# Kernel tuning notes

Measured on AMD Instinct MI355X. Metric: run time of the kernel, lower is better.

The kernel has to match this reference:

```python
import jax, jax.numpy as jnp
import numpy as np

B, S, D, H = 2, 2048, 1024, 16
DEPTH = D // H


def setup_inputs() -> dict:
    key = jax.random.key(0)
    ks = jax.random.split(key, 6)
    q = jax.random.normal(ks[0], (B, S, D), dtype=jnp.float32)
    k = jax.random.normal(ks[1], (B, S, D), dtype=jnp.float32)
    v = jax.random.normal(ks[2], (B, S, D), dtype=jnp.float32)
    # causal mask, broadcastable to [B, H, S, S]
    mask = jnp.tril(jnp.ones((S, S), dtype=bool))[None, None, :, :]
    wq = jax.random.normal(ks[3], (D, D), dtype=jnp.float32)
    wk = jax.random.normal(ks[4], (D, D), dtype=jnp.float32)
    wv = jax.random.normal(ks[5], (D, D), dtype=jnp.float32)
    return {"q": q, "k": k, "v": v, "mask": mask, "wq": wq, "wk": wk, "wv": wv}


def _split_heads(x):
    # [B, S, D] -> [B, H, S, depth]
    return x.reshape(x.shape[0], -1, H, DEPTH).transpose(0, 2, 1, 3)


def reference(q, k, v, mask, wq, wk, wv):
    q = _split_heads(q @ wq)
    k = _split_heads(k @ wk)
    v = _split_heads(v @ wv)
    scale = jnp.sqrt(jnp.float32(DEPTH))
    # [B, H, S, S]
    scores = jnp.einsum("bhqd,bhkd->bhqk", q, k) / scale
    scores = jnp.where(mask, scores, jnp.float32(-8.0))
    scores = scores - jnp.max(scores, axis=-1, keepdims=True)
    attn = jax.nn.softmax(scores, axis=-1)
    out = jnp.einsum("bhqk,bhkd->bhqd", attn, v)
    # [B, H, S, depth] -> [B, S, D]
    return out.transpose(0, 2, 1, 3).reshape(out.shape[0], -1, D)
```

## Files before the change

kernel.cpp:

```cpp
#include <hip/hip_runtime.h>
#include <hip/hip_bf16.h>

#define B_  2
#define S_  2048
#define D_  1024
#define H_  16
#define DH_ 64

typedef __attribute__((ext_vector_type(8)))  short  short8;
typedef __attribute__((ext_vector_type(4)))  short  short4b;
typedef __attribute__((ext_vector_type(16))) float  f32x16;

#define MFMA32(A,B,C) __builtin_amdgcn_mfma_f32_32x32x16_bf16(A,B,C,0,0,0)

static __device__ __forceinline__ short bf16b(float x) {
    __hip_bfloat16 h = __float2bfloat16(x);
    return *(short*)&h;
}
static __device__ __forceinline__ float bf16tof(short s) {
    union { unsigned u; float f; } cv;
    cv.u = ((unsigned)(unsigned short)s) << 16;
    return cv.f;
}
static __device__ __forceinline__ void gl2lds(const short* g, short* l) {
    __builtin_amdgcn_global_load_lds(
        (const __attribute__((address_space(1))) unsigned int*)g,
        (__attribute__((address_space(3))) unsigned int*)l, 16, 0, 0);
}
static __device__ __forceinline__ unsigned cvtpk(float a, float b) {
    unsigned r;
    asm("v_cvt_pk_bf16_f32 %0, %1, %2" : "=v"(r) : "v"(a), "v"(b));
    return r;
}
static __device__ __forceinline__ void pl32swap(unsigned &a, unsigned &b) {
    asm volatile("v_permlane32_swap_b32 %0, %1" : "+v"(a), "+v"(b));
}

__global__ __launch_bounds__(256)
void conv_all(const float* __restrict__ q, const float* __restrict__ k,
              const float* __restrict__ v,
              const float* __restrict__ wq, const float* __restrict__ wk,
              const float* __restrict__ wv, char* __restrict__ ws) {
    __shared__ short HiT[64][80];
    __shared__ short LoT[64][80];
    const int bid = blockIdx.x;
    const int t   = threadIdx.x;
    if (bid < 12288) {
        const int z   = bid >> 12;
        const int xb  = bid & 4095;
        const float* src = z == 0 ? q : z == 1 ? k : v;
        short* hi = (short*)(ws + (size_t)z * 16777216);
        short* lo = hi + 4194304;
        const int i = (xb * 256 + t) * 4;
        float4 xv = *(const float4*)&src[i];
        const float* xf = (const float*)&xv;
        short4b h4, l4;
#pragma unroll
        for (int e = 0; e < 4; ++e) {
            short hb = bf16b(xf[e]);
            h4[e] = hb;
            l4[e] = bf16b(xf[e] - bf16tof(hb));
        }
        *(short4b*)&hi[i] = h4;
        *(short4b*)&lo[i] = l4;
        return;
    }
    const int wid = bid - 12288;
    const int z   = wid >> 8;
    const int rem = wid & 255;
    const int k0  = (rem & 15) << 6, n0 = (rem >> 4) << 6;
    const float* w = z == 0 ? wq : z == 1 ? wk : wv;
    short* oh = (short*)(ws + 50331648 + (size_t)z * 4194304);
    short* ol = oh + 1048576;

    const int kr = t >> 2, c4 = (t & 3) * 16;
    const float* srow = w + (size_t)(k0 + kr) * 1024 + n0 + c4;
#pragma unroll
    for (int u = 0; u < 16; u += 4) {
        float4 f = *(const float4*)&srow[u];
        const float* ff = (const float*)&f;
#pragma unroll
        for (int e = 0; e < 4; ++e) {
            int nl = c4 + u + e;
            short hb = bf16b(ff[e]);
            HiT[nl][kr] = hb;
            LoT[nl][kr] = bf16b(ff[e] - bf16tof(hb));
        }
    }
    __syncthreads();
    const int nl = t >> 2, kc = (t & 3) * 16;
    size_t off = (size_t)(n0 + nl) * 1024 + k0 + kc;
    *(short8*)&oh[off]     = *(const short8*)&HiT[nl][kc];
    *(short8*)&oh[off + 8] = *(const short8*)&HiT[nl][kc + 8];
    *(short8*)&ol[off]     = *(const short8*)&LoT[nl][kc];
    *(short8*)&ol[off + 8] = *(const short8*)&LoT[nl][kc + 8];
}

#define AHI_ 0
#define ALO_ 4096
#define BHI_ 8192
#define BLO_ 12288

__global__ __launch_bounds__(256, 2)
void proj_mfma(const short* __restrict__ xh0, const short* __restrict__ xl0,
               const short* __restrict__ xh1, const short* __restrict__ xl1,
               const short* __restrict__ xh2, const short* __restrict__ xl2,
               const short* __restrict__ wh0, const short* __restrict__ wl0,
               const short* __restrict__ wh1, const short* __restrict__ wl1,
               const short* __restrict__ wh2, const short* __restrict__ wl2,
               short* __restrict__ qh, short* __restrict__ ql,
               short* __restrict__ kh, short* __restrict__ kl,
               short* __restrict__ vt) {
    __shared__ __align__(16) short lds[32768];
    const int z  = blockIdx.z;
    const int m0 = blockIdx.y * 128;
    const int n0 = blockIdx.x * 128;
    const int t = threadIdx.x, lane = t & 63, w = t >> 6;
    const int l31 = lane & 31, hh = lane >> 5;

    const short* xh = z == 0 ? xh0 : z == 1 ? xh1 : xh2;
    const short* xl = z == 0 ? xl0 : z == 1 ? xl1 : xl2;
    const short* wh = z == 0 ? wh0 : z == 1 ? wh1 : wh2;
    const short* wl = z == 0 ? wl0 : z == 1 ? wl1 : wl2;

    const short* gsrc[8];
    short*       ldst[8];
#pragma unroll
    for (int j = 0; j < 8; ++j) {
        int sub = ((j & 1) << 2) | w;
        int cc  = (sub << 6) | lane;
        int row = cc >> 2, p = cc & 3;
        int kc  = p ^ ((row & 3) ^ ((row >> 2) & 3));
        bool isA  = j < 4;
        bool isHi = (j & 2) == 0;
        const short* base = isA ? (isHi ? xh : xl) : (isHi ? wh : wl);
        int r0g = isA ? m0 : n0;
        gsrc[j] = base + (size_t)(r0g + row) * 1024 + kc * 8;
        ldst[j] = &lds[(j >> 1) * 4096 + sub * 512];
    }

    const int rm0 = ((w & 1) << 6) + l31, rm1 = rm0 + 32;
    const int rn0 = ((w >> 1) << 6) + l31, rn1 = rn0 + 32;
    const int swm = (rm0 & 3) ^ ((rm0 >> 2) & 3);
    const int swn = (rn0 & 3) ^ ((rn0 >> 2) & 3);

    f32x16 accs[2][2] = {};

#pragma unroll
    for (int j = 0; j < 8; ++j)
        gl2lds(gsrc[j], ldst[j]);

    for (int kt = 0; kt < 32; ++kt) {
        const int cb = (kt & 1) << 14;
        if (kt < 31) {
            const int nb = 16384 - cb;
#pragma unroll
            for (int j = 0; j < 8; ++j)
                gl2lds(gsrc[j] + (kt + 1) * 32, ldst[j] + nb);
            asm volatile("s_waitcnt vmcnt(8)" ::: "memory");
        } else {
            asm volatile("s_waitcnt vmcnt(0)" ::: "memory");
        }
        __builtin_amdgcn_s_barrier();
        __builtin_amdgcn_sched_barrier(0);
        __builtin_amdgcn_s_setprio(1);
#pragma unroll
        for (int ks = 0; ks < 2; ++ks) {
            const int kc = (ks << 1) | hh;
            const int om = ((kc ^ swm) << 3) + cb;
            const int on = ((kc ^ swn) << 3) + cb;
            short8 ah0 = *(const short8*)&lds[AHI_ + rm0 * 32 + om];
            short8 ah1 = *(const short8*)&lds[AHI_ + rm1 * 32 + om];
            short8 al0 = *(const short8*)&lds[ALO_ + rm0 * 32 + om];
            short8 al1 = *(const short8*)&lds[ALO_ + rm1 * 32 + om];
            short8 bh0 = *(const short8*)&lds[BHI_ + rn0 * 32 + on];
            short8 bh1 = *(const short8*)&lds[BHI_ + rn1 * 32 + on];
            short8 bl0 = *(const short8*)&lds[BLO_ + rn0 * 32 + on];
            short8 bl1 = *(const short8*)&lds[BLO_ + rn1 * 32 + on];
            accs[0][0] = MFMA32(ah0, bh0, accs[0][0]);
            accs[0][1] = MFMA32(ah0, bh1, accs[0][1]);
            accs[1][0] = MFMA32(ah1, bh0, accs[1][0]);
            accs[1][1] = MFMA32(ah1, bh1, accs[1][1]);
            accs[0][0] = MFMA32(ah0, bl0, accs[0][0]);
            accs[0][1] = MFMA32(ah0, bl1, accs[0][1]);
            accs[1][0] = MFMA32(ah1, bl0, accs[1][0]);
            accs[1][1] = MFMA32(ah1, bl1, accs[1][1]);
            accs[0][0] = MFMA32(al0, bh0, accs[0][0]);
            accs[0][1] = MFMA32(al0, bh1, accs[0][1]);
            accs[1][0] = MFMA32(al1, bh0, accs[1][0]);
            accs[1][1] = MFMA32(al1, bh1, accs[1][1]);
        }
        __builtin_amdgcn_s_setprio(0);
        __builtin_amdgcn_sched_barrier(0);
        __builtin_amdgcn_s_barrier();
    }

    const int qm = w & 1, qn = w >> 1;
    const int bb = m0 >> 11;
    const int sbase = (m0 & 2047) + qm * 64;
    if (z < 2) {
        short* oh = z == 0 ? qh : kh;
        short* ol = z == 0 ? ql : kl;
        const float qs = (z == 0) ? 0.125f : 1.0f;
#pragma unroll
        for (int mt = 0; mt < 2; ++mt)
#pragma unroll
        for (int nt = 0; nt < 2; ++nt) {
            int n_g = n0 + qn * 64 + nt * 32 + l31;
            int h = n_g >> 6, d = n_g & 63;
#pragma unroll
            for (int r = 0; r < 16; ++r) {
                int s = sbase + mt * 32 + (r & 3) + 8 * (r >> 2) + 4 * hh;
                size_t off = (((size_t)(bb * 16 + h) * 2048 + s) << 6) + d;
                float a = accs[mt][nt][r] * qs;
                short hb = bf16b(a);
                oh[off] = hb;
                ol[off] = bf16b(a - bf16tof(hb));
            }
        }
    } else {
#pragma unroll
        for (int mt = 0; mt < 2; ++mt)
#pragma unroll
        for (int nt = 0; nt < 2; ++nt) {
            int n_g = n0 + qn * 64 + nt * 32 + l31;
            int h = n_g >> 6, d = n_g & 63;
            size_t vbase = ((size_t)(bb * 16 + h) * 64 + d) * 2048;
#pragma unroll
            for (int r2 = 0; r2 < 4; ++r2) {
                int s0 = sbase + mt * 32 + 8 * r2 + 4 * hh;
                short4b pk;
#pragma unroll
                for (int a2 = 0; a2 < 4; ++a2)
                    pk[a2] = bf16b(accs[mt][nt][r2 * 4 + a2]);
                *(short4b*)&vt[vbase + s0] = pk;
            }
        }
    }
}

__global__ __launch_bounds__(256, 2)
void attn_mfma(const short* __restrict__ Qhi, const short* __restrict__ Qlo,
               const short* __restrict__ Khi, const short* __restrict__ Klo,
               const short* __restrict__ Vt,  float* __restrict__ out) {
    __shared__ __align__(16) short SBUF[24576];
    __shared__ float svp[4][64];
    __shared__ float svs[64];
#define KhiS (SBUF)
#define KloS (SBUF + 8192)
#define VtS  (SBUF + 16384)

    const int t     = threadIdx.x;
    const int lane  = t & 63;
    const int w     = t >> 6;
    const int l31   = lane & 31;
    const int hh    = lane >> 5;
    const int bh    = blockIdx.x;
    const int yy    = blockIdx.y;
    const int qt    = (yy < 8) ? yy : 23 - yy;
    const int q0    = qt * 128;
    const int myq   = q0 + w * 32 + l31;
    const int myq_min = q0 + w * 32;
    const int ktend = 2 * qt + 2;

    const size_t basebh = (size_t)bh * S_ * DH_;

    {
        const int s_begin = ktend * 64;
        float part = 0.f;
        const short* vrow = Vt + basebh + (size_t)lane * S_;
        for (int s = s_begin + w * 8; s < S_; s += 32) {
            short8 vv = *(const short8*)&vrow[s];
#pragma unroll
            for (int e = 0; e < 8; ++e) part += bf16tof(vv[e]);
        }
        svp[w][lane] = part;
    }
    __syncthreads();
    if (t < 64)
        svs[t] = svp[0][t] + svp[1][t] + svp[2][t] + svp[3][t];

    short8 qh[4], ql[4];
    {
        const short* qr = Qhi + basebh + (size_t)myq * DH_;
        const short* lr = Qlo + basebh + (size_t)myq * DH_;
#pragma unroll
        for (int kf = 0; kf < 4; ++kf) {
            int dofs = kf * 16 + hh * 8;
            qh[kf] = *(const short8*)(qr + dofs);
            ql[kf] = *(const short8*)(lr + dofs);
        }
    }

    const int i1 = (w << 6) | lane;
    const int i2 = 256 + i1;
    const int r1 = i1 >> 3, c1 = (i1 & 7) ^ (r1 & 7);
    const int r2 = i2 >> 3, c2 = (i2 & 7) ^ (r2 & 7);
    const short* gKh1 = Khi + basebh + (size_t)r1 * 64 + c1 * 8;
    const short* gKh2 = Khi + basebh + (size_t)r2 * 64 + c2 * 8;
    const short* gKl1 = Klo + basebh + (size_t)r1 * 64 + c1 * 8;
    const short* gKl2 = Klo + basebh + (size_t)r2 * 64 + c2 * 8;
    const short* gV1  = Vt  + basebh + (size_t)r1 * S_ + c1 * 8;
    const short* gV2  = Vt  + basebh + (size_t)r2 * S_ + c2 * 8;
    const int wub = w << 9;

#define ASTAGE(KT, BUF) do {                                                  \
        const int ka_ = (KT) * 4096, va_ = (KT) * 64, bo_ = (BUF) * 4096;     \
        gl2lds(gKh1 + ka_, &KhiS[bo_ + wub]);                                 \
        gl2lds(gKh2 + ka_, &KhiS[bo_ + 2048 + wub]);                          \
        gl2lds(gKl1 + ka_, &KloS[bo_ + wub]);                                 \
        gl2lds(gKl2 + ka_, &KloS[bo_ + 2048 + wub]);                          \
        gl2lds(gV1  + va_, &VtS [bo_ + wub]);                                 \
        gl2lds(gV2  + va_, &VtS [bo_ + 2048 + wub]);                          \
    } while (0)

    float m_run = -INFINITY, l_run = 0.f;
    f32x16 oT0 = {}, oT1 = {};

    const int sw0 = l31 & 7;

    ASTAGE(0, 0);

    for (int kt = 0; kt < ktend; ++kt) {
        const int bo = (kt & 1) << 12;
        asm volatile("s_waitcnt vmcnt(0)" ::: "memory");
        __builtin_amdgcn_s_barrier();
        __builtin_amdgcn_sched_barrier(0);
        if (kt + 1 < ktend)
            ASTAGE(kt + 1, (kt & 1) ^ 1);
        __builtin_amdgcn_sched_barrier(0);

        f32x16 acc0 = {}, acc1 = {};
        __builtin_amdgcn_s_setprio(1);
#pragma unroll
        for (int kf = 0; kf < 4; ++kf) {
            const int cs = ((2 * kf + hh) ^ sw0) << 3;
            short8 k0h = *(const short8*)&KhiS[bo + l31 * 64 + cs];
            short8 k0l = *(const short8*)&KloS[bo + l31 * 64 + cs];
            short8 k1h = *(const short8*)&KhiS[bo + (l31 + 32) * 64 + cs];
            short8 k1l = *(const short8*)&KloS[bo + (l31 + 32) * 64 + cs];
            acc0 = MFMA32(k0h, qh[kf], acc0);
            acc0 = MFMA32(k0h, ql[kf], acc0);
            acc0 = MFMA32(k0l, qh[kf], acc0);
            acc1 = MFMA32(k1h, qh[kf], acc1);
            acc1 = MFMA32(k1h, ql[kf], acc1);
            acc1 = MFMA32(k1l, qh[kf], acc1);
        }
        __builtin_amdgcn_s_setprio(0);

        float vals[32];
        float tmax;
        if (kt * 64 + 63 <= myq_min) {
            float t0 = -INFINITY, t1 = -INFINITY;
#pragma unroll
            for (int r = 0; r < 16; ++r) {
                vals[r]      = acc0[r];
                vals[16 + r] = acc1[r];
                t0 = fmaxf(t0, acc0[r]);
                t1 = fmaxf(t1, acc1[r]);
            }
            tmax = fmaxf(t0, t1);
        } else {
            tmax = -INFINITY;
#pragma unroll
            for (int r = 0; r < 16; ++r) {
                int key0 = kt * 64 + ((r & 3) + 8 * (r >> 2) + 4 * hh);
                float v0 = (key0 <= myq)      ? acc0[r] : -8.0f;
                float v1 = (key0 + 32 <= myq) ? acc1[r] : -8.0f;
                vals[r] = v0;
                vals[16 + r] = v1;
                tmax = fmaxf(tmax, fmaxf(v0, v1));
            }
        }
        tmax = fmaxf(tmax, __shfl_xor(tmax, 32, 64));
        const bool defer = __all(tmax <= m_run + 8.0f);
        if (!defer) {
            float mnew  = fmaxf(m_run, tmax);
            float alpha = __expf(m_run - mnew);
            l_run *= alpha;
#pragma unroll
            for (int r = 0; r < 16; ++r) { oT0[r] *= alpha; oT1[r] *= alpha; }
            m_run = mnew;
        }
        float psum = 0.f;
        unsigned cw[16];
#pragma unroll
        for (int tt = 0; tt < 16; ++tt) {
            float p0 = __expf(vals[2 * tt]     - m_run);
            float p1 = __expf(vals[2 * tt + 1] - m_run);
            psum += p0 + p1;
            cw[tt] = cvtpk(p0, p1);
        }
        psum += __shfl_xor(psum, 32, 64);
        l_run += psum;

        __builtin_amdgcn_s_setprio(1);
#pragma unroll
        for (int kf = 0; kf < 4; ++kf) {
            unsigned w0 = cw[4 * kf],     w1 = cw[4 * kf + 1];
            unsigned w2 = cw[4 * kf + 2], w3 = cw[4 * kf + 3];
            pl32swap(w0, w2);
            pl32swap(w1, w3);
            union { unsigned u[4]; short8 s8; } pu;
            pu.u[0] = w0; pu.u[1] = w1; pu.u[2] = w2; pu.u[3] = w3;
            const int cs = ((2 * kf + hh) ^ sw0) << 3;
            short8 v0 = *(const short8*)&VtS[bo + l31 * 64 + cs];
            short8 v1 = *(const short8*)&VtS[bo + (l31 + 32) * 64 + cs];
            oT0 = MFMA32(v0, pu.s8, oT0);
            oT1 = MFMA32(v1, pu.s8, oT1);
        }
        __builtin_amdgcn_s_setprio(0);
        __builtin_amdgcn_sched_barrier(0);
    }
#undef ASTAGE

    {
        float mfin = fmaxf(m_run, -8.0f);
        float aa   = __expf(m_run - mfin);
        float e8   = __expf(-8.0f - mfin);
        float nrem = (float)(S_ - ktend * 64);
        float lfin = l_run * aa + nrem * e8;
        float inv  = 1.0f / lfin;
#pragma unroll
        for (int r = 0; r < 16; ++r) {
            int dim0 = (r & 3) + 8 * (r >> 2) + 4 * hh;
            oT0[r] = (oT0[r] * aa + e8 * svs[dim0])      * inv;
            oT1[r] = (oT1[r] * aa + e8 * svs[dim0 + 32]) * inv;
        }
    }

    __syncthreads();
    float* Ob = (float*)SBUF + w * 2176;
#pragma unroll
    for (int r = 0; r < 16; ++r) {
        int dim0 = (r & 3) + 8 * (r >> 2) + 4 * hh;
        Ob[l31 * 68 + dim0]      = oT0[r];
        Ob[l31 * 68 + dim0 + 32] = oT1[r];
    }
    {
        const int qq = lane >> 1;
        const int ch = (lane & 1) * 32;
        const float* src = Ob + qq * 68 + ch;
        const int b  = bh >> 4;
        const int h  = bh & 15;
        float* dst = out + ((size_t)b * S_ + (q0 + w * 32 + qq)) * D_ + h * 64 + ch;
#pragma unroll
        for (int c = 0; c < 32; c += 4)
            *(float4*)(dst + c) = *(const float4*)(src + c);
    }
#undef KhiS
#undef KloS
#undef VtS
}

extern "C" void kernel_launch(void* const* d_in, const int* in_sizes, int n_in,
                              void* d_out, int out_size, void* d_ws, size_t ws_size,
                              hipStream_t stream) {
    const float* q  = (const float*)d_in[0];
    const float* k  = (const float*)d_in[1];
    const float* v  = (const float*)d_in[2];
    const float* wq = (const float*)d_in[4];
    const float* wk = (const float*)d_in[5];
    const float* wv = (const float*)d_in[6];
    float* out = (float*)d_out;

    char* ws = (char*)d_ws;
    const short* XH[3] = {(short*)ws, (short*)(ws + 16777216), (short*)(ws + 33554432)};
    const short* XL[3] = {XH[0] + 4194304, XH[1] + 4194304, XH[2] + 4194304};
    const short* WH[3] = {(short*)(ws + 50331648), (short*)(ws + 54525952), (short*)(ws + 58720256)};
    const short* WL[3] = {WH[0] + 1048576, WH[1] + 1048576, WH[2] + 1048576};

    short *Qhi, *Qlo, *Khi, *Klo, *Vt;
    if (ws_size >= (size_t)104857600) {
        Qhi = (short*)(ws + 62914560);
        Qlo = (short*)(ws + 71303168);
        Khi = (short*)(ws + 79691776);
        Klo = (short*)(ws + 88080384);
        Vt  = (short*)(ws + 96468992);
    } else {
        Qhi = (short*)d_in[0]; Qlo = Qhi + 4194304;
        Khi = (short*)d_in[1]; Klo = Khi + 4194304;
        Vt  = (short*)d_in[2];
    }

    conv_all<<<dim3(13056), 256, 0, stream>>>(q, k, v, wq, wk, wv, ws);

    proj_mfma<<<dim3(8, 32, 3), 256, 0, stream>>>(
        XH[0], XL[0], XH[1], XL[1], XH[2], XL[2],
        WH[0], WL[0], WH[1], WL[1], WH[2], WL[2],
        Qhi, Qlo, Khi, Klo, Vt);

    attn_mfma<<<dim3(32, 16), 256, 0, stream>>>(Qhi, Qlo, Khi, Klo, Vt, out);
}
```

Baseline: 270.7 us.

## Single-buffer B operand via registers to cut LDS and raise occupancy

The projection GEMM keeps double-buffered direct-to-LDS loads for the A operand. The B (weight) operand now goes global→register→LDS with a single LDS buffer, so the kernel's LDS drops from 64KB to 48KB and launch bounds ask for 3 blocks per CU instead of 2. The aim is more resident waves to hide latency. In exchange, each iteration gets an extra barrier plus a full vmcnt wait before the B store, so register pressure rises and load latency is less overlapped.

```diff
diff --git a/kernel.cpp b/kernel.cpp
--- a/kernel.cpp
+++ b/kernel.cpp
@@ -98,10 +98,10 @@
 
 #define AHI_ 0
 #define ALO_ 4096
-#define BHI_ 8192
-#define BLO_ 12288
-
-__global__ __launch_bounds__(256, 2)
+#define BHI_ 16384
+#define BLO_ 20480
+
+__global__ __launch_bounds__(256, 3)
 void proj_mfma(const short* __restrict__ xh0, const short* __restrict__ xl0,
                const short* __restrict__ xh1, const short* __restrict__ xl1,
                const short* __restrict__ xh2, const short* __restrict__ xl2,
@@ -111,7 +111,7 @@
                short* __restrict__ qh, short* __restrict__ ql,
                short* __restrict__ kh, short* __restrict__ kl,
                short* __restrict__ vt) {
-    __shared__ __align__(16) short lds[32768];
+    __shared__ __align__(16) short lds[24576];
     const int z  = blockIdx.z;
     const int m0 = blockIdx.y * 128;
     const int n0 = blockIdx.x * 128;
@@ -123,20 +123,28 @@
     const short* wh = z == 0 ? wh0 : z == 1 ? wh1 : wh2;
     const short* wl = z == 0 ? wl0 : z == 1 ? wl1 : wl2;
 
-    const short* gsrc[8];
-    short*       ldst[8];
-#pragma unroll
-    for (int j = 0; j < 8; ++j) {
-        int sub = ((j & 1) << 2) | w;
+    const short* gsrcA[4];
+    short*       ldstA[4];
+#pragma unroll
+    for (int j = 0; j < 4; ++j) {
+        int sub = w + ((j & 1) << 2);
         int cc  = (sub << 6) | lane;
         int row = cc >> 2, p = cc & 3;
         int kc  = p ^ ((row & 3) ^ ((row >> 2) & 3));
-        bool isA  = j < 4;
-        bool isHi = (j & 2) == 0;
-        const short* base = isA ? (isHi ? xh : xl) : (isHi ? wh : wl);
-        int r0g = isA ? m0 : n0;
-        gsrc[j] = base + (size_t)(r0g + row) * 1024 + kc * 8;
-        ldst[j] = &lds[(j >> 1) * 4096 + sub * 512];
+        const short* base = (j < 2) ? xh : xl;
+        gsrcA[j] = base + (size_t)(m0 + row) * 1024 + kc * 8;
+        ldstA[j] = &lds[((j < 2) ? AHI_ : ALO_) + sub * 512];
+    }
+    const short* gsrcB[4];
+    int ldsoB[4];
+#pragma unroll
+    for (int m = 0; m < 4; ++m) {
+        int cc  = t + ((m & 1) << 8);
+        int row = cc >> 2, p = cc & 3;
+        int sw  = (row & 3) ^ ((row >> 2) & 3);
+        const short* base = (m < 2) ? wh : wl;
+        gsrcB[m] = base + (size_t)(n0 + row) * 1024 + p * 8;
+        ldsoB[m] = ((m < 2) ? BHI_ : BLO_) + row * 32 + (p ^ sw) * 8;
     }
 
     const int rm0 = ((w & 1) << 6) + l31, rm1 = rm0 + 32;
@@ -145,30 +153,40 @@
     const int swn = (rn0 & 3) ^ ((rn0 >> 2) & 3);
 
     f32x16 accs[2][2] = {};
-
-#pragma unroll
-    for (int j = 0; j < 8; ++j)
-        gl2lds(gsrc[j], ldst[j]);
+    short8 breg[4];
+
+#pragma unroll
+    for (int j = 0; j < 4; ++j)
+        gl2lds(gsrcA[j], ldstA[j]);
+#pragma unroll
+    for (int m = 0; m < 4; ++m)
+        breg[m] = *(const short8*)(gsrcB[m]);
+    asm volatile("s_waitcnt vmcnt(0)" ::: "memory");
+#pragma unroll
+    for (int m = 0; m < 4; ++m)
+        *(short8*)&lds[ldsoB[m]] = breg[m];
 
     for (int kt = 0; kt < 32; ++kt) {
-        const int cb = (kt & 1) << 14;
+        const int cb = (kt & 1) << 13;
+        asm volatile("s_waitcnt lgkmcnt(0)" ::: "memory");
+        __builtin_amdgcn_s_barrier();
+        __builtin_amdgcn_sched_barrier(0);
         if (kt < 31) {
-            const int nb = 16384 - cb;
-#pragma unroll
-            for (int j = 0; j < 8; ++j)
-                gl2lds(gsrc[j] + (kt + 1) * 32, ldst[j] + nb);
-            asm volatile("s_waitcnt vmcnt(8)" ::: "memory");
-        } else {
-            asm volatile("s_waitcnt vmcnt(0)" ::: "memory");
-        }
-        __builtin_amdgcn_s_barrier();
+            const int ab = ((kt + 1) & 1) << 13;
+#pragma unroll
+            for (int j = 0; j < 4; ++j)
+                gl2lds(gsrcA[j] + (kt + 1) * 32, ldstA[j] + ab);
+#pragma unroll
+            for (int m = 0; m < 4; ++m)
+                breg[m] = *(const short8*)(gsrcB[m] + (kt + 1) * 32);
+        }
         __builtin_amdgcn_sched_barrier(0);
         __builtin_amdgcn_s_setprio(1);
 #pragma unroll
         for (int ks = 0; ks < 2; ++ks) {
             const int kc = (ks << 1) | hh;
             const int om = ((kc ^ swm) << 3) + cb;
-            const int on = ((kc ^ swn) << 3) + cb;
+            const int on = (kc ^ swn) << 3;
             short8 ah0 = *(const short8*)&lds[AHI_ + rm0 * 32 + om];
             short8 ah1 = *(const short8*)&lds[AHI_ + rm1 * 32 + om];
             short8 al0 = *(const short8*)&lds[ALO_ + rm0 * 32 + om];
@@ -193,6 +211,12 @@
         __builtin_amdgcn_s_setprio(0);
         __builtin_amdgcn_sched_barrier(0);
         __builtin_amdgcn_s_barrier();
+        if (kt < 31) {
+            asm volatile("s_waitcnt vmcnt(0)" ::: "memory");
+#pragma unroll
+            for (int m = 0; m < 4; ++m)
+                *(short8*)&lds[ldsoB[m]] = breg[m];
+        }
     }
 
     const int qm = w & 1, qn = w >> 1;
```

Result: no change. 275.6 us (+1.8%).

## Enlarge projection GEMM tile to 256x256 with 8 waves and phased prefetch

Applied to the files above, without the earlier changes.

Restructures the QKV projection kernel from 128x128 tiles with 4 waves to 256x256 tiles with 8 waves and 128KB of LDS. The K loop now runs in four phases, each interleaving LDS fragment loads, partial global-to-LDS prefetch of the next stage and a block of MFMAs. The LDS layout uses a new 2-way swizzle over 16-wide k slices. The aim is more operand reuse per loaded byte and better overlap of loads with MFMA work. The cost is 192 blocks instead of 768, which may underfill the GPU, and more barriers per iteration.

```diff
diff --git a/kernel.cpp b/kernel.cpp
--- a/kernel.cpp
+++ b/kernel.cpp
@@ -96,12 +96,12 @@
     *(short8*)&ol[off + 8] = *(const short8*)&LoT[nl][kc + 8];
 }
 
-#define AHI_ 0
-#define ALO_ 4096
-#define BHI_ 8192
-#define BLO_ 12288
-
-__global__ __launch_bounds__(256, 2)
+#define QAH_ 0
+#define QAL_ 4096
+#define QBH_ 8192
+#define QBL_ 12288
+
+__global__ __launch_bounds__(512, 2)
 void proj_mfma(const short* __restrict__ xh0, const short* __restrict__ xl0,
                const short* __restrict__ xh1, const short* __restrict__ xl1,
                const short* __restrict__ xh2, const short* __restrict__ xl2,
@@ -111,108 +111,164 @@
                short* __restrict__ qh, short* __restrict__ ql,
                short* __restrict__ kh, short* __restrict__ kl,
                short* __restrict__ vt) {
-    __shared__ __align__(16) short lds[32768];
+    __shared__ __align__(16) short lds[65536];
     const int z  = blockIdx.z;
-    const int m0 = blockIdx.y * 128;
-    const int n0 = blockIdx.x * 128;
+    const int m0 = blockIdx.y * 256;
+    const int n0 = blockIdx.x * 256;
     const int t = threadIdx.x, lane = t & 63, w = t >> 6;
     const int l31 = lane & 31, hh = lane >> 5;
+    const int wr = w >> 2, wc = w & 3;
 
     const short* xh = z == 0 ? xh0 : z == 1 ? xh1 : xh2;
     const short* xl = z == 0 ? xl0 : z == 1 ? xl1 : xl2;
     const short* wh = z == 0 ? wh0 : z == 1 ? wh1 : wh2;
     const short* wl = z == 0 ? wl0 : z == 1 ? wl1 : wl2;
 
-    const short* gsrc[8];
-    short*       ldst[8];
-#pragma unroll
-    for (int j = 0; j < 8; ++j) {
-        int sub = ((j & 1) << 2) | w;
-        int cc  = (sub << 6) | lane;
-        int row = cc >> 2, p = cc & 3;
-        int kc  = p ^ ((row & 3) ^ ((row >> 2) & 3));
-        bool isA  = j < 4;
-        bool isHi = (j & 2) == 0;
-        const short* base = isA ? (isHi ? xh : xl) : (isHi ? wh : wl);
-        int r0g = isA ? m0 : n0;
-        gsrc[j] = base + (size_t)(r0g + row) * 1024 + kc * 8;
-        ldst[j] = &lds[(j >> 1) * 4096 + sub * 512];
-    }
-
-    const int rm0 = ((w & 1) << 6) + l31, rm1 = rm0 + 32;
-    const int rn0 = ((w >> 1) << 6) + l31, rn1 = rn0 + 32;
-    const int swm = (rm0 & 3) ^ ((rm0 >> 2) & 3);
-    const int swn = (rn0 & 3) ^ ((rn0 >> 2) & 3);
-
-    f32x16 accs[2][2] = {};
-
-#pragma unroll
-    for (int j = 0; j < 8; ++j)
-        gl2lds(gsrc[j], ldst[j]);
+    const int c    = (w << 6) | lane;
+    const int rowS = c >> 1, pq = c & 1;
+    const int pqs8 = (pq ^ ((rowS >> 2) & 1)) * 8;
+    const short* gAh = xh + (size_t)(m0 + rowS) * 1024 + pqs8;
+    const short* gAl = xl + (size_t)(m0 + rowS) * 1024 + pqs8;
+    const short* gBh = wh + (size_t)(n0 + rowS) * 1024 + pqs8;
+    const short* gBl = wl + (size_t)(n0 + rowS) * 1024 + pqs8;
+    const int wS = w << 9;
+
+    const int co = ((hh ^ ((l31 >> 2) & 1)) << 3);
+    int rA[4], rB[2];
+#pragma unroll
+    for (int p = 0; p < 4; ++p) rA[p] = (wr * 128 + p * 32 + l31) * 16 + co;
+#pragma unroll
+    for (int n = 0; n < 2; ++n) rB[n] = (wc * 64 + n * 32 + l31) * 16 + co;
+
+    f32x16 acc[4][2] = {};
+
+    gl2lds(gAh,      &lds[QAH_ + wS]);
+    gl2lds(gBh,      &lds[QBH_ + wS]);
+    gl2lds(gAl,      &lds[QAL_ + wS]);
+    gl2lds(gBl,      &lds[QBL_ + wS]);
+    gl2lds(gAh + 16, &lds[16384 + QAH_ + wS]);
+    gl2lds(gBh + 16, &lds[16384 + QBH_ + wS]);
+    gl2lds(gAl + 16, &lds[16384 + QAL_ + wS]);
+    gl2lds(gBl + 16, &lds[16384 + QBL_ + wS]);
+    asm volatile("s_waitcnt vmcnt(4)" ::: "memory");
+    __builtin_amdgcn_s_barrier();
+
+#define PHASE_MFMA(PA, PB)                                                    \
+    acc[PA][0] = MFMA32(ah0, bh0k, acc[PA][0]);                               \
+    acc[PA][1] = MFMA32(ah0, bh1k, acc[PA][1]);                               \
+    acc[PB][0] = MFMA32(ah1, bh0k, acc[PB][0]);                               \
+    acc[PB][1] = MFMA32(ah1, bh1k, acc[PB][1]);                               \
+    acc[PA][0] = MFMA32(ah0, bl0k, acc[PA][0]);                               \
+    acc[PA][1] = MFMA32(ah0, bl1k, acc[PA][1]);                               \
+    acc[PB][0] = MFMA32(ah1, bl0k, acc[PB][0]);                               \
+    acc[PB][1] = MFMA32(ah1, bl1k, acc[PB][1]);                               \
+    acc[PA][0] = MFMA32(al0, bh0k, acc[PA][0]);                               \
+    acc[PA][1] = MFMA32(al0, bh1k, acc[PA][1]);                               \
+    acc[PB][0] = MFMA32(al1, bh0k, acc[PB][0]);                               \
+    acc[PB][1] = MFMA32(al1, bh1k, acc[PB][1]);
 
     for (int kt = 0; kt < 32; ++kt) {
-        const int cb = (kt & 1) << 14;
-        if (kt < 31) {
-            const int nb = 16384 - cb;
-#pragma unroll
-            for (int j = 0; j < 8; ++j)
-                gl2lds(gsrc[j] + (kt + 1) * 32, ldst[j] + nb);
-            asm volatile("s_waitcnt vmcnt(8)" ::: "memory");
-        } else {
-            asm volatile("s_waitcnt vmcnt(0)" ::: "memory");
-        }
-        __builtin_amdgcn_s_barrier();
+        const int tb = (kt & 1) << 15;
+        const int nb = 32768 - tb;
+        const int nk = (kt + 1) * 32;
+        const bool st = (kt < 31);
+
+        short8 bh0k, bh1k, bl0k, bl1k, ah0, ah1, al0, al1;
+
+        __builtin_amdgcn_sched_barrier(0);
+        bh0k = *(const short8*)&lds[tb + QBH_ + rB[0]];
+        bh1k = *(const short8*)&lds[tb + QBH_ + rB[1]];
+        bl0k = *(const short8*)&lds[tb + QBL_ + rB[0]];
+        bl1k = *(const short8*)&lds[tb + QBL_ + rB[1]];
+        ah0  = *(const short8*)&lds[tb + QAH_ + rA[0]];
+        ah1  = *(const short8*)&lds[tb + QAH_ + rA[1]];
+        al0  = *(const short8*)&lds[tb + QAL_ + rA[0]];
+        al1  = *(const short8*)&lds[tb + QAL_ + rA[1]];
+        if (st) { gl2lds(gAh + nk, &lds[nb + QAH_ + wS]);
+                  gl2lds(gBh + nk, &lds[nb + QBH_ + wS]); }
+        __builtin_amdgcn_s_barrier();
+        asm volatile("s_waitcnt lgkmcnt(0)" ::: "memory");
         __builtin_amdgcn_sched_barrier(0);
         __builtin_amdgcn_s_setprio(1);
-#pragma unroll
-        for (int ks = 0; ks < 2; ++ks) {
-            const int kc = (ks << 1) | hh;
-            const int om = ((kc ^ swm) << 3) + cb;
-            const int on = ((kc ^ swn) << 3) + cb;
-            short8 ah0 = *(const short8*)&lds[AHI_ + rm0 * 32 + om];
-            short8 ah1 = *(const short8*)&lds[AHI_ + rm1 * 32 + om];
-            short8 al0 = *(const short8*)&lds[ALO_ + rm0 * 32 + om];
-            short8 al1 = *(const short8*)&lds[ALO_ + rm1 * 32 + om];
-            short8 bh0 = *(const short8*)&lds[BHI_ + rn0 * 32 + on];
-            short8 bh1 = *(const short8*)&lds[BHI_ + rn1 * 32 + on];
-            short8 bl0 = *(const short8*)&lds[BLO_ + rn0 * 32 + on];
-            short8 bl1 = *(const short8*)&lds[BLO_ + rn1 * 32 + on];
-            accs[0][0] = MFMA32(ah0, bh0, accs[0][0]);
-            accs[0][1] = MFMA32(ah0, bh1, accs[0][1]);
-            accs[1][0] = MFMA32(ah1, bh0, accs[1][0]);
-            accs[1][1] = MFMA32(ah1, bh1, accs[1][1]);
-            accs[0][0] = MFMA32(ah0, bl0, accs[0][0]);
-            accs[0][1] = MFMA32(ah0, bl1, accs[0][1]);
-            accs[1][0] = MFMA32(ah1, bl0, accs[1][0]);
-            accs[1][1] = MFMA32(ah1, bl1, accs[1][1]);
-            accs[0][0] = MFMA32(al0, bh0, accs[0][0]);
-            accs[0][1] = MFMA32(al0, bh1, accs[0][1]);
-            accs[1][0] = MFMA32(al1, bh0, accs[1][0]);
-            accs[1][1] = MFMA32(al1, bh1, accs[1][1]);
-        }
+        PHASE_MFMA(0, 1)
         __builtin_amdgcn_s_setprio(0);
         __builtin_amdgcn_sched_barrier(0);
         __builtin_amdgcn_s_barrier();
-    }
-
-    const int qm = w & 1, qn = w >> 1;
+
+        __builtin_amdgcn_sched_barrier(0);
+        ah0 = *(const short8*)&lds[tb + QAH_ + rA[2]];
+        ah1 = *(const short8*)&lds[tb + QAH_ + rA[3]];
+        al0 = *(const short8*)&lds[tb + QAL_ + rA[2]];
+        al1 = *(const short8*)&lds[tb + QAL_ + rA[3]];
+        if (st) { gl2lds(gAl + nk, &lds[nb + QAL_ + wS]);
+                  gl2lds(gBl + nk, &lds[nb + QBL_ + wS]);
+                  asm volatile("s_waitcnt vmcnt(4)" ::: "memory");
+        } else {  asm volatile("s_waitcnt vmcnt(0)" ::: "memory"); }
+        __builtin_amdgcn_s_barrier();
+        asm volatile("s_waitcnt lgkmcnt(0)" ::: "memory");
+        __builtin_amdgcn_sched_barrier(0);
+        __builtin_amdgcn_s_setprio(1);
+        PHASE_MFMA(2, 3)
+        __builtin_amdgcn_s_setprio(0);
+        __builtin_amdgcn_sched_barrier(0);
+        __builtin_amdgcn_s_barrier();
+
+        __builtin_amdgcn_sched_barrier(0);
+        bh0k = *(const short8*)&lds[tb + 16384 + QBH_ + rB[0]];
+        bh1k = *(const short8*)&lds[tb + 16384 + QBH_ + rB[1]];
+        bl0k = *(const short8*)&lds[tb + 16384 + QBL_ + rB[0]];
+        bl1k = *(const short8*)&lds[tb + 16384 + QBL_ + rB[1]];
+        ah0  = *(const short8*)&lds[tb + 16384 + QAH_ + rA[0]];
+        ah1  = *(const short8*)&lds[tb + 16384 + QAH_ + rA[1]];
+        al0  = *(const short8*)&lds[tb + 16384 + QAL_ + rA[0]];
+        al1  = *(const short8*)&lds[tb + 16384 + QAL_ + rA[1]];
+        if (st) { gl2lds(gAh + nk + 16, &lds[nb + 16384 + QAH_ + wS]);
+                  gl2lds(gBh + nk + 16, &lds[nb + 16384 + QBH_ + wS]); }
+        __builtin_amdgcn_s_barrier();
+        asm volatile("s_waitcnt lgkmcnt(0)" ::: "memory");
+        __builtin_amdgcn_sched_barrier(0);
+        __builtin_amdgcn_s_setprio(1);
+        PHASE_MFMA(0, 1)
+        __builtin_amdgcn_s_setprio(0);
+        __builtin_amdgcn_sched_barrier(0);
+        __builtin_amdgcn_s_barrier();
+
+        __builtin_amdgcn_sched_barrier(0);
+        ah0 = *(const short8*)&lds[tb + 16384 + QAH_ + rA[2]];
+        ah1 = *(const short8*)&lds[tb + 16384 + QAH_ + rA[3]];
+        al0 = *(const short8*)&lds[tb + 16384 + QAL_ + rA[2]];
+        al1 = *(const short8*)&lds[tb + 16384 + QAL_ + rA[3]];
+        if (st) { gl2lds(gAl + nk + 16, &lds[nb + 16384 + QAL_ + wS]);
+                  gl2lds(gBl + nk + 16, &lds[nb + 16384 + QBL_ + wS]);
+                  asm volatile("s_waitcnt vmcnt(4)" ::: "memory"); }
+        __builtin_amdgcn_s_barrier();
+        asm volatile("s_waitcnt lgkmcnt(0)" ::: "memory");
+        __builtin_amdgcn_sched_barrier(0);
+        __builtin_amdgcn_s_setprio(1);
+        PHASE_MFMA(2, 3)
+        __builtin_amdgcn_s_setprio(0);
+        __builtin_amdgcn_sched_barrier(0);
+        __builtin_amdgcn_s_barrier();
+    }
+#undef PHASE_MFMA
+
     const int bb = m0 >> 11;
-    const int sbase = (m0 & 2047) + qm * 64;
+    const int sbase = (m0 & 2047) + wr * 128;
     if (z < 2) {
         short* oh = z == 0 ? qh : kh;
         short* ol = z == 0 ? ql : kl;
         const float qs = (z == 0) ? 0.125f : 1.0f;
 #pragma unroll
-        for (int mt = 0; mt < 2; ++mt)
+        for (int p = 0; p < 4; ++p)
 #pragma unroll
         for (int nt = 0; nt < 2; ++nt) {
-            int n_g = n0 + qn * 64 + nt * 32 + l31;
+            int n_g = n0 + wc * 64 + nt * 32 + l31;
             int h = n_g >> 6, d = n_g & 63;
 #pragma unroll
             for (int r = 0; r < 16; ++r) {
-                int s = sbase + mt * 32 + (r & 3) + 8 * (r >> 2) + 4 * hh;
+                int s = sbase + p * 32 + (r & 3) + 8 * (r >> 2) + 4 * hh;
                 size_t off = (((size_t)(bb * 16 + h) * 2048 + s) << 6) + d;
-                float a = accs[mt][nt][r] * qs;
+                float a = acc[p][nt][r] * qs;
                 short hb = bf16b(a);
                 oh[off] = hb;
                 ol[off] = bf16b(a - bf16tof(hb));
@@ -220,19 +276,19 @@
         }
     } else {
 #pragma unroll
-        for (int mt = 0; mt < 2; ++mt)
+        for (int p = 0; p < 4; ++p)
 #pragma unroll
         for (int nt = 0; nt < 2; ++nt) {
-            int n_g = n0 + qn * 64 + nt * 32 + l31;
+            int n_g = n0 + wc * 64 + nt * 32 + l31;
             int h = n_g >> 6, d = n_g & 63;
             size_t vbase = ((size_t)(bb * 16 + h) * 64 + d) * 2048;
 #pragma unroll
             for (int r2 = 0; r2 < 4; ++r2) {
-                int s0 = sbase + mt * 32 + 8 * r2 + 4 * hh;
+                int s0 = sbase + p * 32 + 8 * r2 + 4 * hh;
                 short4b pk;
 #pragma unroll
                 for (int a2 = 0; a2 < 4; ++a2)
-                    pk[a2] = bf16b(accs[mt][nt][r2 * 4 + a2]);
+                    pk[a2] = bf16b(acc[p][nt][r2 * 4 + a2]);
                 *(short4b*)&vt[vbase + s0] = pk;
             }
         }
@@ -485,7 +541,7 @@
 
     conv_all<<<dim3(13056), 256, 0, stream>>>(q, k, v, wq, wk, wv, ws);
 
-    proj_mfma<<<dim3(8, 32, 3), 256, 0, stream>>>(
+    proj_mfma<<<dim3(4, 16, 3), 512, 0, stream>>>(
         XH[0], XL[0], XH[1], XL[1], XH[2], XL[2],
         WH[0], WL[0], WH[1], WL[1], WH[2], WL[2],
         Qhi, Qlo, Khi, Klo, Vt);
```

After: 267.3 us. No clear change (-1.3%).
